# Kernel tuning notes

Hardware: AMD Instinct MI355X
Metric: run time of the kernel (lower is better)

The kernel has to match this reference:

```python
import jax, jax.numpy as jnp
import numpy as np

C = 128  # in_dim = hidden_dim = out_dim = vector_dim
K = 16   # n_sample neighbors


def setup_inputs() -> dict:
    key = jax.random.key(0)
    ks = jax.random.split(key, 16)
    B, N = 4, 4096
    d = {}
    d["input_p"] = jax.random.normal(ks[0], (B, 3, N), jnp.float32)
    d["input_x"] = jax.random.normal(ks[1], (B, C, N), jnp.float32)

    def W(k_, o, i):
        return jax.random.normal(k_, (o, i), jnp.float32) * (1.0 / np.sqrt(i))

    # 1x1 conv weights (out,in) + biases
    specs = [("top", C), ("phi", C), ("psi", C), ("alpha", C), ("d1", 3),
             ("d2", C), ("g1", C), ("g2", C), ("down", C)]
    for j, (n, i) in enumerate(specs):
        d["W_" + n] = W(ks[2 + j], C, i)
        d["b_" + n] = jnp.zeros((C,), jnp.float32)
    # folded eval-mode BatchNorm: per-channel scale / shift
    for j, n in enumerate(["top", "d1", "d2", "g1", "g2", "down"]):
        kk = jax.random.fold_in(key, 100 + j)
        d["s_" + n] = 1.0 + 0.1 * jax.random.normal(kk, (C,), jnp.float32)
        d["t_" + n] = 0.1 * jax.random.normal(jax.random.fold_in(kk, 1), (C,), jnp.float32)
    return d


def _lin(x, Wm, b):
    # 1x1 conv == per-point linear; x: [..., in], Wm: [out, in]
    return jnp.einsum('oi,...i->...o', Wm, x) + b


def _bn(x, s, t):
    return x * s + t


def _forward(input_p, input_x,
             W_top, b_top, W_phi, b_phi, W_psi, b_psi, W_alpha, b_alpha,
             W_d1, b_d1, W_d2, b_d2, W_g1, b_g1, W_g2, b_g2, W_down, b_down,
             s_top, t_top, s_d1, t_d1, s_d2, t_d2, s_g1, t_g1, s_g2, t_g2,
             s_down, t_down):
    p = jnp.transpose(input_p, (0, 2, 1))   # [B,N,3]
    x = jnp.transpose(input_x, (0, 2, 1))   # [B,N,C]

    # ---- KNN: k nearest (squared euclidean, self included) ----
    sq = jnp.sum(p * p, -1)                                  # [B,N]
    d2 = sq[:, :, None] + sq[:, None, :] - 2.0 * jnp.einsum('bnd,bmd->bnm', p, p)
    _, idx = jax.lax.top_k(-d2, K)                           # [B,N,K]

    gather = jax.vmap(lambda f, i: f[i])                     # -> [B,N,K,feat]

    # ---- linear_top (conv1d + BN) ----
    top = _bn(_lin(x, W_top, b_top), s_top, t_top)           # [B,N,C]
    phi = _lin(top, W_phi, b_phi)                            # [B,N,C] (query)
    psi = _lin(top, W_psi, b_psi)                            # keys
    alp = _lin(top, W_alpha, b_alpha)                        # values

    psi_n = gather(psi, idx)                                 # [B,N,K,C]
    alp_n = gather(alp, idx)                                 # [B,N,K,C]
    p_n = gather(p, idx)                                     # [B,N,K,3]

    # ---- delta: positional encoding MLP on relative xyz ----
    rel = p[:, :, None, :] - p_n                             # [B,N,K,3]
    h = jax.nn.relu(_bn(_lin(rel, W_d1, b_d1), s_d1, t_d1))
    delta = _bn(_lin(h, W_d2, b_d2), s_d2, t_d2)             # [B,N,K,C]

    # ---- gamma: vector attention logits MLP ----
    g = phi[:, :, None, :] - psi_n + delta                   # [B,N,K,C]
    g = jax.nn.relu(_bn(_lin(g, W_g1, b_g1), s_g1, t_g1))
    g = _bn(_lin(g, W_g2, b_g2), s_g2, t_g2)                 # [B,N,K,C]

    attn = jax.nn.softmax(g, axis=2)                         # softmax over K neighbors
    y = jnp.sum(attn * (alp_n + delta), axis=2)              # [B,N,C]

    out = _bn(_lin(y, W_down, b_down), s_down, t_down) + x   # residual
    return jnp.transpose(out, (0, 2, 1))                     # [B,C,N]


def reference(input_p, input_x,
              W_top, b_top, W_phi, b_phi, W_psi, b_psi, W_alpha, b_alpha,
              W_d1, b_d1, W_d2, b_d2, W_g1, b_g1, W_g2, b_g2, W_down, b_down,
              s_top, t_top, s_d1, t_d1, s_d2, t_d2, s_g1, t_g1, s_g2, t_g2,
              s_down, t_down):
    return _forward(input_p, input_x,
                    W_top, b_top, W_phi, b_phi, W_psi, b_psi, W_alpha, b_alpha,
                    W_d1, b_d1, W_d2, b_d2, W_g1, b_g1, W_g2, b_g2,
                    W_down, b_down,
                    s_top, t_top, s_d1, t_d1, s_d2, t_d2, s_g1, t_g1,
                    s_g2, t_g2, s_down, t_down)
```

## Files before the change

kernel.cpp:

```cpp
#include <hip/hip_runtime.h>
#include <math.h>


#define NPTS 4096
#define BATCH 4
#define CDIM 128
#define KNBR 16
#define SA 68

__device__ __forceinline__ void load8(const float* __restrict__ v, int c0, float (&o)[8]) {
    float4 a = *(const float4*)&v[c0];
    float4 b = *(const float4*)&v[c0 + 4];
    o[0]=a.x; o[1]=a.y; o[2]=a.z; o[3]=a.w; o[4]=b.x; o[5]=b.y; o[6]=b.z; o[7]=b.w;
}

__device__ __forceinline__ void stage_wt(const float* __restrict__ gW, float* __restrict__ sW, int t) {
    const int kq = t & 31;
    const int cq0 = t >> 5;
    #pragma unroll
    for (int r = 0; r < 4; ++r) {
        const int c0 = (cq0 + r * 8) * 4;
        const int k0 = kq * 4;
        float4 w0 = *(const float4*)&gW[(c0+0)*128 + k0];
        float4 w1 = *(const float4*)&gW[(c0+1)*128 + k0];
        float4 w2 = *(const float4*)&gW[(c0+2)*128 + k0];
        float4 w3 = *(const float4*)&gW[(c0+3)*128 + k0];
        const float r0[4] = {w0.x,w0.y,w0.z,w0.w};
        const float r1[4] = {w1.x,w1.y,w1.z,w1.w};
        const float r2[4] = {w2.x,w2.y,w2.z,w2.w};
        const float r3[4] = {w3.x,w3.y,w3.z,w3.w};
        #pragma unroll
        for (int j = 0; j < 4; ++j) {
            const int k = k0 + j;
            float4 v = make_float4(r0[j], r1[j], r2[j], r3[j]);
            *(float4*)&sW[k*128 + (c0 ^ (k & 0x7C))] = v;
        }
    }
}

__device__ __forceinline__ void gemm128(const float* __restrict__ sIn, const float* __restrict__ sW,
                                        int r0, int c0, float (&acc)[4][8]) {
    #pragma unroll 4
    for (int k = 0; k < 128; ++k) {
        float4 a = *(const float4*)&sIn[k*SA + r0];
        const int sw = k & 0x7C;
        float4 b0 = *(const float4*)&sW[k*128 + (c0 ^ sw)];
        float4 b1 = *(const float4*)&sW[k*128 + ((c0+4) ^ sw)];
        const float av[4] = {a.x, a.y, a.z, a.w};
        const float bv[8] = {b0.x,b0.y,b0.z,b0.w,b1.x,b1.y,b1.z,b1.w};
        #pragma unroll
        for (int i = 0; i < 4; ++i)
            #pragma unroll
            for (int j = 0; j < 8; ++j)
                acc[i][j] = fmaf(av[i], bv[j], acc[i][j]);
    }
}

__device__ __forceinline__ void write_colmajor(float* __restrict__ sDst, int r0, int c0,
                                               const float (&v)[4][8]) {
    #pragma unroll
    for (int j = 0; j < 8; ++j) {
        float4 q = make_float4(v[0][j], v[1][j], v[2][j], v[3][j]);
        *(float4*)&sDst[(c0 + j)*SA + r0] = q;
    }
}

template<bool RELU>
__device__ __forceinline__ void epi_bn(float (&acc)[4][8], const float* __restrict__ bias,
                                       const float* __restrict__ sc, const float* __restrict__ sh, int c0) {
    float bb[8], ss[8], tt[8];
    load8(bias, c0, bb); load8(sc, c0, ss); load8(sh, c0, tt);
    #pragma unroll
    for (int i = 0; i < 4; ++i)
        #pragma unroll
        for (int j = 0; j < 8; ++j) {
            float v = fmaf(acc[i][j] + bb[j], ss[j], tt[j]);
            if (RELU) v = fmaxf(v, 0.f);
            acc[i][j] = v;
        }
}

__device__ __forceinline__ void epi_bias(float (&acc)[4][8], const float* __restrict__ bias, int c0) {
    float bb[8]; load8(bias, c0, bb);
    #pragma unroll
    for (int i = 0; i < 4; ++i)
        #pragma unroll
        for (int j = 0; j < 8; ++j) acc[i][j] += bb[j];
}

__device__ __forceinline__ void store_rows(float* __restrict__ dst, int b, int n0, int r0, int c0,
                                           const float (&v)[4][8]) {
    #pragma unroll
    for (int i = 0; i < 4; ++i) {
        float* row = &dst[((size_t)b*NPTS + n0 + r0 + i)*CDIM + c0];
        *(float4*)row     = make_float4(v[i][0], v[i][1], v[i][2], v[i][3]);
        *(float4*)(row+4) = make_float4(v[i][4], v[i][5], v[i][6], v[i][7]);
    }
}

__global__ __launch_bounds__(512)
void knn_kernel(const float* __restrict__ p, int* __restrict__ idx_out) {
    __shared__ float4 p4[NPTS];
    __shared__ float  mv[8*16*64];
    __shared__ int    mi[8*16*64];
    const int b = blockIdx.y, n0 = blockIdx.x*64, t = threadIdx.x;
    const float* pb = p + (size_t)b*3*NPTS;
    for (int m = t; m < NPTS; m += 512) {
        float xx = pb[m], yy = pb[NPTS+m], zz = pb[2*NPTS+m];
        p4[m] = make_float4(xx, yy, zz, xx*xx + yy*yy + zz*zz);
    }
    __syncthreads();
    const int w = t >> 6, l = t & 63;
    const float4 Q = p4[n0 + l];
    float bv[16]; int bi[16];
    #pragma unroll
    for (int j = 0; j < 16; ++j) { bv[j] = __builtin_inff(); bi[j] = 0x7FFFFFFF; }
    const int m0 = w * 512;
    for (int mm = 0; mm < 512; ++mm) {
        const int m = m0 + mm;
        const float4 P = p4[m];
        float dot = Q.x * P.x;
        dot = fmaf(Q.y, P.y, dot);
        dot = fmaf(Q.z, P.z, dot);
        const float d2 = fmaf(-2.f, dot, Q.w + P.w);
        if (d2 < bv[15]) {
            float cv = d2; int ci = m;
            #pragma unroll
            for (int j = 0; j < 16; ++j) {
                bool s_ = (cv < bv[j]) || (cv == bv[j] && ci < bi[j]);
                float tv = bv[j]; int ti = bi[j];
                bv[j] = s_ ? cv : tv;  bi[j] = s_ ? ci : ti;
                cv    = s_ ? tv : cv;  ci    = s_ ? ti : ci;
            }
        }
    }
    #pragma unroll
    for (int j = 0; j < 16; ++j) { mv[(w*16+j)*64 + l] = bv[j]; mi[(w*16+j)*64 + l] = bi[j]; }
    __syncthreads();
    if (t < 64) {
        const int q = t;
        float av[16]; int ai[16];
        #pragma unroll
        for (int j = 0; j < 16; ++j) { av[j] = mv[j*64+q]; ai[j] = mi[j*64+q]; }
        for (int w2 = 1; w2 < 8; ++w2) {
            float bw[16]; int bidx[16];
            #pragma unroll
            for (int j = 0; j < 16; ++j) { bw[j] = mv[(w2*16+j)*64+q]; bidx[j] = mi[(w2*16+j)*64+q]; }
            float cv[16]; int ci[16];
            #pragma unroll
            for (int j = 0; j < 16; ++j) {
                float a1 = av[j]; int a2 = ai[j];
                float b1 = bw[15-j]; int b2 = bidx[15-j];
                bool lt = (a1 < b1) || (a1 == b1 && a2 < b2);
                cv[j] = lt ? a1 : b1; ci[j] = lt ? a2 : b2;
            }
            #pragma unroll
            for (int gap = 8; gap >= 1; gap >>= 1) {
                #pragma unroll
                for (int i = 0; i < 16; ++i) {
                    if ((i & gap) == 0) {
                        const int k2 = i + gap;
                        bool le = (cv[i] < cv[k2]) || (cv[i] == cv[k2] && ci[i] < ci[k2]);
                        float tv = cv[i], tw = cv[k2]; int ti = ci[i], tj = ci[k2];
                        cv[i]  = le ? tv : tw; ci[i]  = le ? ti : tj;
                        cv[k2] = le ? tw : tv; ci[k2] = le ? tj : ti;
                    }
                }
            }
            #pragma unroll
            for (int j = 0; j < 16; ++j) { av[j] = cv[j]; ai[j] = ci[j]; }
        }
        int* orow = &idx_out[((size_t)b*NPTS + n0 + q)*KNBR];
        #pragma unroll
        for (int j = 0; j < 16; ++j) orow[j] = ai[j];
    }
}

__global__ __launch_bounds__(256)
void top_proj_kernel(const float* __restrict__ x,
                     const float* __restrict__ Wt_, const float* __restrict__ bt_,
                     const float* __restrict__ st_, const float* __restrict__ tt_,
                     const float* __restrict__ Wph, const float* __restrict__ bph,
                     const float* __restrict__ Wps, const float* __restrict__ bps,
                     const float* __restrict__ Wal, const float* __restrict__ bal,
                     float* __restrict__ phi, float* __restrict__ psi, float* __restrict__ alp) {
    __shared__ float sX[128*SA];
    __shared__ float sT[128*SA];
    __shared__ float sW[128*128];
    const int t = threadIdx.x, tx = t & 15, ty = t >> 4;
    const int r0 = tx*4, c0 = ty*8;
    const int b = blockIdx.y, n0 = blockIdx.x*64;
    #pragma unroll
    for (int rr = 0; rr < 8; ++rr) {
        const int k = rr*16 + ty;
        *(float4*)&sX[k*SA + r0] = *(const float4*)&x[((size_t)b*CDIM + k)*NPTS + n0 + r0];
    }
    stage_wt(Wt_, sW, t);
    __syncthreads();
    {
        float acc[4][8] = {};
        gemm128(sX, sW, r0, c0, acc);
        epi_bn<false>(acc, bt_, st_, tt_, c0);
        write_colmajor(sT, r0, c0, acc);
    }
    __syncthreads();
    stage_wt(Wph, sW, t); __syncthreads();
    { float a2[4][8] = {}; gemm128(sT, sW, r0, c0, a2); epi_bias(a2, bph, c0); store_rows(phi, b, n0, r0, c0, a2); }
    __syncthreads();
    stage_wt(Wps, sW, t); __syncthreads();
    { float a2[4][8] = {}; gemm128(sT, sW, r0, c0, a2); epi_bias(a2, bps, c0); store_rows(psi, b, n0, r0, c0, a2); }
    __syncthreads();
    stage_wt(Wal, sW, t); __syncthreads();
    { float a2[4][8] = {}; gemm128(sT, sW, r0, c0, a2); epi_bias(a2, bal, c0); store_rows(alp, b, n0, r0, c0, a2); }
}

__global__ __launch_bounds__(256)
void pt_attn_kernel(const float* __restrict__ p,
                    const float* __restrict__ phi, const float* __restrict__ psi,
                    const float* __restrict__ alp, const int* __restrict__ idx,
                    const float* __restrict__ W_d1, const float* __restrict__ b_d1,
                    const float* __restrict__ W_d2, const float* __restrict__ b_d2,
                    const float* __restrict__ W_g1, const float* __restrict__ b_g1,
                    const float* __restrict__ W_g2, const float* __restrict__ b_g2,
                    const float* __restrict__ s_d1, const float* __restrict__ t_d1,
                    const float* __restrict__ s_d2, const float* __restrict__ t_d2,
                    const float* __restrict__ s_g1, const float* __restrict__ t_g1,
                    const float* __restrict__ s_g2, const float* __restrict__ t_g2,
                    float* __restrict__ yT) {
    __shared__ float sA[128*SA];
    __shared__ float sB[128*SA];
    __shared__ float sW[128*128];
    __shared__ float sWd1[3*128];
    __shared__ float sRel[3*SA];
    __shared__ float sPhi[4*132];
    __shared__ int   sIdx[64];
    const int t = threadIdx.x, tx = t & 15, ty = t >> 4;
    const int r0 = tx*4, c0 = ty*8;
    const int b = blockIdx.y, n0 = blockIdx.x*4;

    if (t < 64) sIdx[t] = idx[((size_t)b*NPTS + n0 + (t >> 4))*KNBR + (t & 15)];
    if (t < 128) {
        const int pt_ = t >> 5, cq = t & 31;
        *(float4*)&sPhi[pt_*132 + cq*4] = *(const float4*)&phi[((size_t)b*NPTS + n0 + pt_)*CDIM + cq*4];
    }
    if (t >= 128) {
        const int c = t - 128;
        #pragma unroll
        for (int j = 0; j < 3; ++j) sWd1[j*128 + c] = W_d1[c*3 + j];
    }
    __syncthreads();
    if (t < 192) {
        const int j = t / 64, r = t % 64;
        const float pq = p[((size_t)b*3 + j)*NPTS + n0 + (r >> 4)];
        const float pn = p[((size_t)b*3 + j)*NPTS + sIdx[r]];
        sRel[j*SA + r] = pq - pn;
    }
    stage_wt(W_d2, sW, t);
    __syncthreads();
    {
        float acc[4][8] = {};
        #pragma unroll
        for (int k = 0; k < 3; ++k) {
            float4 a = *(const float4*)&sRel[k*SA + r0];
            float bv8[8]; load8(&sWd1[k*128], c0, bv8);
            const float av[4] = {a.x, a.y, a.z, a.w};
            #pragma unroll
            for (int i = 0; i < 4; ++i)
                #pragma unroll
                for (int j = 0; j < 8; ++j) acc[i][j] = fmaf(av[i], bv8[j], acc[i][j]);
        }
        epi_bn<true>(acc, b_d1, s_d1, t_d1, c0);
        write_colmajor(sA, r0, c0, acc);
    }
    __syncthreads();
    float dl[4][8];
    {
        float acc[4][8] = {};
        gemm128(sA, sW, r0, c0, acc);
        epi_bn<false>(acc, b_d2, s_d2, t_d2, c0);
        #pragma unroll
        for (int i = 0; i < 4; ++i)
            #pragma unroll
            for (int j = 0; j < 8; ++j) dl[i][j] = acc[i][j];
    }
    __syncthreads();
    {
        const int pt_ = tx >> 2;
        float ph[8]; load8(&sPhi[pt_*132], c0, ph);
        float g0[4][8];
        #pragma unroll
        for (int i = 0; i < 4; ++i) {
            const int jn = sIdx[r0 + i];
            float ps[8]; load8(&psi[((size_t)b*NPTS + jn)*CDIM], c0, ps);
            #pragma unroll
            for (int j = 0; j < 8; ++j) g0[i][j] = ph[j] - ps[j] + dl[i][j];
        }
        write_colmajor(sA, r0, c0, g0);
        stage_wt(W_g1, sW, t);
    }
    __syncthreads();
    {
        float acc[4][8] = {};
        gemm128(sA, sW, r0, c0, acc);
        epi_bn<true>(acc, b_g1, s_g1, t_g1, c0);
        write_colmajor(sB, r0, c0, acc);
    }
    __syncthreads();
    stage_wt(W_g2, sW, t);
    __syncthreads();
    float g2[4][8] = {};
    gemm128(sB, sW, r0, c0, g2);
    epi_bn<false>(g2, b_g2, s_g2, t_g2, c0);
    float den[8];
    #pragma unroll
    for (int j = 0; j < 8; ++j) {
        float m_ = fmaxf(fmaxf(g2[0][j], g2[1][j]), fmaxf(g2[2][j], g2[3][j]));
        m_ = fmaxf(m_, __shfl_xor(m_, 1));
        m_ = fmaxf(m_, __shfl_xor(m_, 2));
        float s_ = 0.f;
        #pragma unroll
        for (int i = 0; i < 4; ++i) { g2[i][j] = __expf(g2[i][j] - m_); s_ += g2[i][j]; }
        s_ += __shfl_xor(s_, 1);
        s_ += __shfl_xor(s_, 2);
        den[j] = s_;
    }
    float ya[8] = {};
    #pragma unroll
    for (int i = 0; i < 4; ++i) {
        const int jn = sIdx[r0 + i];
        float al[8]; load8(&alp[((size_t)b*NPTS + jn)*CDIM], c0, al);
        #pragma unroll
        for (int j = 0; j < 8; ++j) ya[j] = fmaf(g2[i][j], al[j] + dl[i][j], ya[j]);
    }
    #pragma unroll
    for (int j = 0; j < 8; ++j) {
        ya[j] += __shfl_xor(ya[j], 1);
        ya[j] += __shfl_xor(ya[j], 2);
    }
    if ((tx & 3) == 0) {
        const int pt_ = tx >> 2;
        #pragma unroll
        for (int j = 0; j < 8; ++j)
            yT[((size_t)b*CDIM + c0 + j)*NPTS + n0 + pt_] = ya[j] / den[j];
    }
}

__global__ __launch_bounds__(256)
void down_kernel(const float* __restrict__ yT, const float* __restrict__ x,
                 const float* __restrict__ Wd, const float* __restrict__ bd,
                 const float* __restrict__ sd, const float* __restrict__ td,
                 float* __restrict__ out) {
    __shared__ float sY[128*SA];
    __shared__ float sW[128*128];
    const int t = threadIdx.x, tx = t & 15, ty = t >> 4;
    const int r0 = tx*4, c0 = ty*8;
    const int b = blockIdx.y, n0 = blockIdx.x*64;
    #pragma unroll
    for (int rr = 0; rr < 8; ++rr) {
        const int k = rr*16 + ty;
        *(float4*)&sY[k*SA + r0] = *(const float4*)&yT[((size_t)b*CDIM + k)*NPTS + n0 + r0];
    }
    stage_wt(Wd, sW, t);
    __syncthreads();
    float acc[4][8] = {};
    gemm128(sY, sW, r0, c0, acc);
    epi_bn<false>(acc, bd, sd, td, c0);
    #pragma unroll
    for (int j = 0; j < 8; ++j) {
        const float* xrow = &x[((size_t)b*CDIM + c0 + j)*NPTS + n0 + r0];
        float4 res = *(const float4*)xrow;
        float4 o = make_float4(acc[0][j] + res.x, acc[1][j] + res.y,
                               acc[2][j] + res.z, acc[3][j] + res.w);
        *(float4*)&out[((size_t)b*CDIM + c0 + j)*NPTS + n0 + r0] = o;
    }
}

extern "C" void kernel_launch(void* const* d_in, const int* in_sizes, int n_in,
                              void* d_out, int out_size, void* d_ws, size_t ws_size,
                              hipStream_t stream) {
    const float* p    = (const float*)d_in[0];
    const float* x    = (const float*)d_in[1];
    const float* Wtop = (const float*)d_in[2];  const float* btop = (const float*)d_in[3];
    const float* Wphi = (const float*)d_in[4];  const float* bphi = (const float*)d_in[5];
    const float* Wpsi = (const float*)d_in[6];  const float* bpsi = (const float*)d_in[7];
    const float* Walp = (const float*)d_in[8];  const float* balp = (const float*)d_in[9];
    const float* Wd1  = (const float*)d_in[10]; const float* bd1  = (const float*)d_in[11];
    const float* Wd2  = (const float*)d_in[12]; const float* bd2  = (const float*)d_in[13];
    const float* Wg1  = (const float*)d_in[14]; const float* bg1  = (const float*)d_in[15];
    const float* Wg2  = (const float*)d_in[16]; const float* bg2  = (const float*)d_in[17];
    const float* Wdn  = (const float*)d_in[18]; const float* bdn  = (const float*)d_in[19];
    const float* stop = (const float*)d_in[20]; const float* ttop = (const float*)d_in[21];
    const float* sd1  = (const float*)d_in[22]; const float* td1  = (const float*)d_in[23];
    const float* sd2  = (const float*)d_in[24]; const float* td2  = (const float*)d_in[25];
    const float* sg1  = (const float*)d_in[26]; const float* tg1  = (const float*)d_in[27];
    const float* sg2  = (const float*)d_in[28]; const float* tg2  = (const float*)d_in[29];
    const float* sdn  = (const float*)d_in[30]; const float* tdn  = (const float*)d_in[31];

    char* ws = (char*)d_ws;
    int*   idx = (int*)ws;
    float* phi = (float*)(ws + (1 << 20));
    float* psi = phi + (size_t)BATCH*NPTS*CDIM;
    float* alp = psi + (size_t)BATCH*NPTS*CDIM;
    float* yT  = alp + (size_t)BATCH*NPTS*CDIM;

    dim3 gk(NPTS/64, BATCH);
    knn_kernel<<<gk, 512, 0, stream>>>(p, idx);
    dim3 g1(NPTS/64, BATCH);
    top_proj_kernel<<<g1, 256, 0, stream>>>(x, Wtop, btop, stop, ttop,
                                            Wphi, bphi, Wpsi, bpsi, Walp, balp,
                                            phi, psi, alp);
    dim3 g2(NPTS/4, BATCH);
    pt_attn_kernel<<<g2, 256, 0, stream>>>(p, phi, psi, alp, idx,
                                           Wd1, bd1, Wd2, bd2, Wg1, bg1, Wg2, bg2,
                                           sd1, td1, sd2, td2, sg1, tg1, sg2, tg2, yT);
    dim3 g3(NPTS/64, BATCH);
    down_kernel<<<g3, 256, 0, stream>>>(yT, x, Wdn, bdn, sdn, tdn, (float*)d_out);
}
```

Measured before the change: 1.089 ms.

## Halve shared-memory weight staging and reuse activation buffers to raise occupancy

Each 128x128 weight is now staged in two 64-row halves, and the separate intermediate activation buffers are dropped in favour of writing back into the input buffer. This cuts per-block LDS roughly in half so two blocks per CU fit, declared through launch_bounds(256,2). The cost is extra __syncthreads and twice as many staging phases per GEMM. The KNN insertion also drops the index tie-break comparison, which can change the chosen neighbour order when distances are exactly equal.

```diff
diff --git a/kernel.cpp b/kernel.cpp
--- a/kernel.cpp
+++ b/kernel.cpp
@@ -14,38 +14,39 @@
     o[0]=a.x; o[1]=a.y; o[2]=a.z; o[3]=a.w; o[4]=b.x; o[5]=b.y; o[6]=b.z; o[7]=b.w;
 }
 
-__device__ __forceinline__ void stage_wt(const float* __restrict__ gW, float* __restrict__ sW, int t) {
-    const int kq = t & 31;
-    const int cq0 = t >> 5;
-    #pragma unroll
-    for (int r = 0; r < 4; ++r) {
-        const int c0 = (cq0 + r * 8) * 4;
-        const int k0 = kq * 4;
-        float4 w0 = *(const float4*)&gW[(c0+0)*128 + k0];
-        float4 w1 = *(const float4*)&gW[(c0+1)*128 + k0];
-        float4 w2 = *(const float4*)&gW[(c0+2)*128 + k0];
-        float4 w3 = *(const float4*)&gW[(c0+3)*128 + k0];
-        const float r0[4] = {w0.x,w0.y,w0.z,w0.w};
-        const float r1[4] = {w1.x,w1.y,w1.z,w1.w};
-        const float r2[4] = {w2.x,w2.y,w2.z,w2.w};
-        const float r3[4] = {w3.x,w3.y,w3.z,w3.w};
+__device__ __forceinline__ void stage_wt_half(const float* __restrict__ gW, float* __restrict__ sW,
+                                              int t, int k0) {
+    const int kq = t & 15;
+    const int cg = t >> 4;
+    #pragma unroll
+    for (int r = 0; r < 2; ++r) {
+        const int c0 = (cg + r * 16) * 4;
+        const int kk = kq * 4;
+        float4 w0 = *(const float4*)&gW[(c0+0)*128 + k0 + kk];
+        float4 w1 = *(const float4*)&gW[(c0+1)*128 + k0 + kk];
+        float4 w2 = *(const float4*)&gW[(c0+2)*128 + k0 + kk];
+        float4 w3 = *(const float4*)&gW[(c0+3)*128 + k0 + kk];
+        const float r0v[4] = {w0.x,w0.y,w0.z,w0.w};
+        const float r1v[4] = {w1.x,w1.y,w1.z,w1.w};
+        const float r2v[4] = {w2.x,w2.y,w2.z,w2.w};
+        const float r3v[4] = {w3.x,w3.y,w3.z,w3.w};
         #pragma unroll
         for (int j = 0; j < 4; ++j) {
-            const int k = k0 + j;
-            float4 v = make_float4(r0[j], r1[j], r2[j], r3[j]);
-            *(float4*)&sW[k*128 + (c0 ^ (k & 0x7C))] = v;
-        }
-    }
-}
-
-__device__ __forceinline__ void gemm128(const float* __restrict__ sIn, const float* __restrict__ sW,
-                                        int r0, int c0, float (&acc)[4][8]) {
+            const int kl = kk + j;
+            float4 v = make_float4(r0v[j], r1v[j], r2v[j], r3v[j]);
+            *(float4*)&sW[kl*128 + (c0 ^ (kl & 0x7C))] = v;
+        }
+    }
+}
+
+__device__ __forceinline__ void gemm64(const float* __restrict__ sIn, const float* __restrict__ sW,
+                                       int r0, int c0, float (&acc)[4][8]) {
     #pragma unroll 4
-    for (int k = 0; k < 128; ++k) {
-        float4 a = *(const float4*)&sIn[k*SA + r0];
-        const int sw = k & 0x7C;
-        float4 b0 = *(const float4*)&sW[k*128 + (c0 ^ sw)];
-        float4 b1 = *(const float4*)&sW[k*128 + ((c0+4) ^ sw)];
+    for (int kl = 0; kl < 64; ++kl) {
+        float4 a = *(const float4*)&sIn[kl*SA + r0];
+        const int sw = kl & 0x7C;
+        float4 b0 = *(const float4*)&sW[kl*128 + (c0 ^ sw)];
+        float4 b1 = *(const float4*)&sW[kl*128 + ((c0+4) ^ sw)];
         const float av[4] = {a.x, a.y, a.z, a.w};
         const float bv[8] = {b0.x,b0.y,b0.z,b0.w,b1.x,b1.y,b1.z,b1.w};
         #pragma unroll
@@ -127,7 +128,7 @@
             float cv = d2; int ci = m;
             #pragma unroll
             for (int j = 0; j < 16; ++j) {
-                bool s_ = (cv < bv[j]) || (cv == bv[j] && ci < bi[j]);
+                bool s_ = (cv < bv[j]);
                 float tv = bv[j]; int ti = bi[j];
                 bv[j] = s_ ? cv : tv;  bi[j] = s_ ? ci : ti;
                 cv    = s_ ? tv : cv;  ci    = s_ ? ti : ci;
@@ -176,7 +177,7 @@
     }
 }
 
-__global__ __launch_bounds__(256)
+__global__ __launch_bounds__(256, 2)
 void top_proj_kernel(const float* __restrict__ x,
                      const float* __restrict__ Wt_, const float* __restrict__ bt_,
                      const float* __restrict__ st_, const float* __restrict__ tt_,
@@ -185,8 +186,7 @@
                      const float* __restrict__ Wal, const float* __restrict__ bal,
                      float* __restrict__ phi, float* __restrict__ psi, float* __restrict__ alp) {
     __shared__ float sX[128*SA];
-    __shared__ float sT[128*SA];
-    __shared__ float sW[128*128];
+    __shared__ float sW[64*128];
     const int t = threadIdx.x, tx = t & 15, ty = t >> 4;
     const int r0 = tx*4, c0 = ty*8;
     const int b = blockIdx.y, n0 = blockIdx.x*64;
@@ -195,26 +195,45 @@
         const int k = rr*16 + ty;
         *(float4*)&sX[k*SA + r0] = *(const float4*)&x[((size_t)b*CDIM + k)*NPTS + n0 + r0];
     }
-    stage_wt(Wt_, sW, t);
+    stage_wt_half(Wt_, sW, t, 0);
+    __syncthreads();
+    float topv[4][8] = {};
+    gemm64(sX, sW, r0, c0, topv);
+    __syncthreads();
+    stage_wt_half(Wt_, sW, t, 64);
+    __syncthreads();
+    gemm64(sX + 64*SA, sW, r0, c0, topv);
+    epi_bn<false>(topv, bt_, st_, tt_, c0);
+    __syncthreads();
+    write_colmajor(sX, r0, c0, topv);
+    stage_wt_half(Wph, sW, t, 0);
     __syncthreads();
     {
-        float acc[4][8] = {};
-        gemm128(sX, sW, r0, c0, acc);
-        epi_bn<false>(acc, bt_, st_, tt_, c0);
-        write_colmajor(sT, r0, c0, acc);
-    }
-    __syncthreads();
-    stage_wt(Wph, sW, t); __syncthreads();
-    { float a2[4][8] = {}; gemm128(sT, sW, r0, c0, a2); epi_bias(a2, bph, c0); store_rows(phi, b, n0, r0, c0, a2); }
-    __syncthreads();
-    stage_wt(Wps, sW, t); __syncthreads();
-    { float a2[4][8] = {}; gemm128(sT, sW, r0, c0, a2); epi_bias(a2, bps, c0); store_rows(psi, b, n0, r0, c0, a2); }
-    __syncthreads();
-    stage_wt(Wal, sW, t); __syncthreads();
-    { float a2[4][8] = {}; gemm128(sT, sW, r0, c0, a2); epi_bias(a2, bal, c0); store_rows(alp, b, n0, r0, c0, a2); }
-}
-
-__global__ __launch_bounds__(256)
+        float a2[4][8] = {};
+        gemm64(sX, sW, r0, c0, a2);
+        __syncthreads(); stage_wt_half(Wph, sW, t, 64); __syncthreads();
+        gemm64(sX + 64*SA, sW, r0, c0, a2);
+        epi_bias(a2, bph, c0); store_rows(phi, b, n0, r0, c0, a2);
+    }
+    __syncthreads(); stage_wt_half(Wps, sW, t, 0); __syncthreads();
+    {
+        float a2[4][8] = {};
+        gemm64(sX, sW, r0, c0, a2);
+        __syncthreads(); stage_wt_half(Wps, sW, t, 64); __syncthreads();
+        gemm64(sX + 64*SA, sW, r0, c0, a2);
+        epi_bias(a2, bps, c0); store_rows(psi, b, n0, r0, c0, a2);
+    }
+    __syncthreads(); stage_wt_half(Wal, sW, t, 0); __syncthreads();
+    {
+        float a2[4][8] = {};
+        gemm64(sX, sW, r0, c0, a2);
+        __syncthreads(); stage_wt_half(Wal, sW, t, 64); __syncthreads();
+        gemm64(sX + 64*SA, sW, r0, c0, a2);
+        epi_bias(a2, bal, c0); store_rows(alp, b, n0, r0, c0, a2);
+    }
+}
+
+__global__ __launch_bounds__(256, 2)
 void pt_attn_kernel(const float* __restrict__ p,
                     const float* __restrict__ phi, const float* __restrict__ psi,
                     const float* __restrict__ alp, const int* __restrict__ idx,
@@ -228,8 +247,7 @@
                     const float* __restrict__ s_g2, const float* __restrict__ t_g2,
                     float* __restrict__ yT) {
     __shared__ float sA[128*SA];
-    __shared__ float sB[128*SA];
-    __shared__ float sW[128*128];
+    __shared__ float sW[64*128];
     __shared__ float sWd1[3*128];
     __shared__ float sRel[3*SA];
     __shared__ float sPhi[4*132];
@@ -248,6 +266,7 @@
         #pragma unroll
         for (int j = 0; j < 3; ++j) sWd1[j*128 + c] = W_d1[c*3 + j];
     }
+    stage_wt_half(W_d2, sW, t, 0);
     __syncthreads();
     if (t < 192) {
         const int j = t / 64, r = t % 64;
@@ -255,7 +274,6 @@
         const float pn = p[((size_t)b*3 + j)*NPTS + sIdx[r]];
         sRel[j*SA + r] = pq - pn;
     }
-    stage_wt(W_d2, sW, t);
     __syncthreads();
     {
         float acc[4][8] = {};
@@ -273,16 +291,13 @@
         write_colmajor(sA, r0, c0, acc);
     }
     __syncthreads();
-    float dl[4][8];
-    {
-        float acc[4][8] = {};
-        gemm128(sA, sW, r0, c0, acc);
-        epi_bn<false>(acc, b_d2, s_d2, t_d2, c0);
-        #pragma unroll
-        for (int i = 0; i < 4; ++i)
-            #pragma unroll
-            for (int j = 0; j < 8; ++j) dl[i][j] = acc[i][j];
-    }
+    float dl[4][8] = {};
+    gemm64(sA, sW, r0, c0, dl);
+    __syncthreads();
+    stage_wt_half(W_d2, sW, t, 64);
+    __syncthreads();
+    gemm64(sA + 64*SA, sW, r0, c0, dl);
+    epi_bn<false>(dl, b_d2, s_d2, t_d2, c0);
     __syncthreads();
     {
         const int pt_ = tx >> 2;
@@ -296,20 +311,26 @@
             for (int j = 0; j < 8; ++j) g0[i][j] = ph[j] - ps[j] + dl[i][j];
         }
         write_colmajor(sA, r0, c0, g0);
-        stage_wt(W_g1, sW, t);
-    }
-    __syncthreads();
-    {
-        float acc[4][8] = {};
-        gemm128(sA, sW, r0, c0, acc);
-        epi_bn<true>(acc, b_g1, s_g1, t_g1, c0);
-        write_colmajor(sB, r0, c0, acc);
-    }
-    __syncthreads();
-    stage_wt(W_g2, sW, t);
+        stage_wt_half(W_g1, sW, t, 0);
+    }
+    __syncthreads();
+    float g1[4][8] = {};
+    gemm64(sA, sW, r0, c0, g1);
+    __syncthreads();
+    stage_wt_half(W_g1, sW, t, 64);
+    __syncthreads();
+    gemm64(sA + 64*SA, sW, r0, c0, g1);
+    epi_bn<true>(g1, b_g1, s_g1, t_g1, c0);
+    __syncthreads();
+    write_colmajor(sA, r0, c0, g1);
+    stage_wt_half(W_g2, sW, t, 0);
     __syncthreads();
     float g2[4][8] = {};
-    gemm128(sB, sW, r0, c0, g2);
+    gemm64(sA, sW, r0, c0, g2);
+    __syncthreads();
+    stage_wt_half(W_g2, sW, t, 64);
+    __syncthreads();
+    gemm64(sA + 64*SA, sW, r0, c0, g2);
     epi_bn<false>(g2, b_g2, s_g2, t_g2, c0);
     float den[8];
     #pragma unroll
@@ -345,13 +366,13 @@
     }
 }
 
-__global__ __launch_bounds__(256)
+__global__ __launch_bounds__(256, 2)
 void down_kernel(const float* __restrict__ yT, const float* __restrict__ x,
                  const float* __restrict__ Wd, const float* __restrict__ bd,
                  const float* __restrict__ sd, const float* __restrict__ td,
                  float* __restrict__ out) {
     __shared__ float sY[128*SA];
-    __shared__ float sW[128*128];
+    __shared__ float sW[64*128];
     const int t = threadIdx.x, tx = t & 15, ty = t >> 4;
     const int r0 = tx*4, c0 = ty*8;
     const int b = blockIdx.y, n0 = blockIdx.x*64;
@@ -360,10 +381,14 @@
         const int k = rr*16 + ty;
         *(float4*)&sY[k*SA + r0] = *(const float4*)&yT[((size_t)b*CDIM + k)*NPTS + n0 + r0];
     }
-    stage_wt(Wd, sW, t);
+    stage_wt_half(Wd, sW, t, 0);
     __syncthreads();
     float acc[4][8] = {};
-    gemm128(sY, sW, r0, c0, acc);
+    gemm64(sY, sW, r0, c0, acc);
+    __syncthreads();
+    stage_wt_half(Wd, sW, t, 64);
+    __syncthreads();
+    gemm64(sY + 64*SA, sW, r0, c0, acc);
     epi_bn<false>(acc, bd, sd, td, c0);
     #pragma unroll
     for (int j = 0; j < 8; ++j) {
@@ -383,7 +408,7 @@
     const float* Wtop = (const float*)d_in[2];  const float* btop = (const float*)d_in[3];
     const float* Wphi = (const float*)d_in[4];  const float* bphi = (const float*)d_in[5];
     const float* Wpsi = (const float*)d_in[6];  const float* bpsi = (const float*)d_in[7];
-    const float* Walp = (const float*)d_in[8];  const float* balp = (const float*)d_in[9];
+    const float* Wal  = (const float*)d_in[8];  const float* bal  = (const float*)d_in[9];
     const float* Wd1  = (const float*)d_in[10]; const float* bd1  = (const float*)d_in[11];
     const float* Wd2  = (const float*)d_in[12]; const float* bd2  = (const float*)d_in[13];
     const float* Wg1  = (const float*)d_in[14]; const float* bg1  = (const float*)d_in[15];
@@ -407,7 +432,7 @@
     knn_kernel<<<gk, 512, 0, stream>>>(p, idx);
     dim3 g1(NPTS/64, BATCH);
     top_proj_kernel<<<g1, 256, 0, stream>>>(x, Wtop, btop, stop, ttop,
-                                            Wphi, bphi, Wpsi, bpsi, Walp, balp,
+                                            Wphi, bphi, Wpsi, bpsi, Wal, bal,
                                             phi, psi, alp);
     dim3 g2(NPTS/4, BATCH);
     pt_attn_kernel<<<g2, 256, 0, stream>>>(p, phi, psi, alp, idx,
```

After: 1.006 ms. -7.6%, faster.
